# Kernel tuning notes

Measured on AMD Instinct MI355X. Metric: run time of the kernel, lower is better.

The kernel has to match this reference:

```python
import jax, jax.numpy as jnp
import numpy as np

N = 50000      # nodes
E = 640000     # edges
F_IN = 64      # node feature dim
H = 128        # hidden channels
G = 256        # graphs in batch
NEG_SLOPE = 0.2
BN_EPS = 1e-5


def setup_inputs() -> dict:
    key = jax.random.key(0)
    ks = jax.random.split(key, 32)
    rn = lambda k, shape, s=0.1: jax.random.normal(k, shape, dtype=jnp.float32) * s
    inp = {
        'x': jax.random.normal(ks[0], (N, F_IN), dtype=jnp.float32),
        'edge_index': jax.random.randint(ks[1], (2, E), 0, N, dtype=jnp.int32),
        'batch': jnp.sort(jax.random.randint(ks[2], (N,), 0, G, dtype=jnp.int32)),
        # GATConv 1
        'W1': rn(ks[3], (F_IN, H)), 'as1': rn(ks[4], (H,)), 'ad1': rn(ks[5], (H,)), 'b1': jnp.zeros((H,), jnp.float32),
        # GATConv 2
        'W2': rn(ks[6], (H, H)), 'as2': rn(ks[7], (H,)), 'ad2': rn(ks[8], (H,)), 'b2': jnp.zeros((H,), jnp.float32),
        # GATConv 3
        'W3': rn(ks[9], (H, H)), 'as3': rn(ks[10], (H,)), 'ad3': rn(ks[11], (H,)), 'b3': jnp.zeros((H,), jnp.float32),
        # BatchNorm (inference: running stats)
        'g1': jnp.ones((H,), jnp.float32), 'be1': jnp.zeros((H,), jnp.float32), 'm1': rn(ks[12], (H,), 0.01), 'v1': jnp.ones((H,), jnp.float32),
        'g2': jnp.ones((H,), jnp.float32), 'be2': jnp.zeros((H,), jnp.float32), 'm2': rn(ks[13], (H,), 0.01), 'v2': jnp.ones((H,), jnp.float32),
        'g3': jnp.ones((H,), jnp.float32), 'be3': jnp.zeros((H,), jnp.float32), 'm3': rn(ks[14], (H,), 0.01), 'v3': jnp.ones((H,), jnp.float32),
        # MLP head
        'lw1': rn(ks[15], (H, H)), 'lb1': jnp.zeros((H,), jnp.float32),
        'lw2': rn(ks[16], (H, 1)), 'lb2': jnp.zeros((1,), jnp.float32),
    }
    return inp


def gat_layer(x, src, dst, W, a_src, a_dst, b, n):
    # PyG GATConv, heads=1: linear, per-edge attention, segment softmax over dst, scatter-add.
    h = x @ W                                  # [N, H]
    s_src = h @ a_src                          # [N]
    s_dst = h @ a_dst                          # [N]
    e = jax.nn.leaky_relu(s_src[src] + s_dst[dst], NEG_SLOPE)   # [E']
    m = jax.ops.segment_max(e, dst, num_segments=n)
    ex = jnp.exp(e - m[dst])
    denom = jax.ops.segment_sum(ex, dst, num_segments=n)
    coef = ex / denom[dst]                     # softmax per destination node
    out = jax.ops.segment_sum(coef[:, None] * h[src], dst, num_segments=n)
    return out + b


def batch_norm(x, g, b, mean, var):
    return (x - mean) * jax.lax.rsqrt(var + BN_EPS) * g + b


def reference(x, edge_index, batch,
              W1, as1, ad1, b1, W2, as2, ad2, b2, W3, as3, ad3, b3,
              g1, be1, m1, v1, g2, be2, m2, v2, g3, be3, m3, v3,
              lw1, lb1, lw2, lb2):
    n = x.shape[0]
    loops = jnp.arange(n, dtype=edge_index.dtype)      # PyG adds self-loops by default
    src = jnp.concatenate([edge_index[0], loops])
    dst = jnp.concatenate([edge_index[1], loops])

    h = gat_layer(x, src, dst, W1, as1, ad1, b1, n)
    h = jax.nn.relu(batch_norm(h, g1, be1, m1, v1))
    h = gat_layer(h, src, dst, W2, as2, ad2, b2, n)
    h = jax.nn.relu(batch_norm(h, g2, be2, m2, v2))
    h = gat_layer(h, src, dst, W3, as3, ad3, b3, n)
    h = jax.nn.relu(batch_norm(h, g3, be3, m3, v3))

    # global_mean_pool
    counts = jax.ops.segment_sum(jnp.ones((n,), h.dtype), batch, num_segments=G)
    pooled = jax.ops.segment_sum(h, batch, num_segments=G) / jnp.maximum(counts, 1.0)[:, None]

    out = jax.nn.relu(pooled @ lw1 + lb1)
    out = out @ lw2 + lb2                               # [G, 1]
    return out
```

## Files before the change

kernel.cpp:

```cpp
#include <hip/hip_runtime.h>

#define HD 128
#define NEG 0.2f
#define BNEPS 1e-5f
#define BSH 11
#define NBSLOT 32

typedef unsigned int uint32;
typedef __attribute__((ext_vector_type(8))) short short8;
typedef __attribute__((ext_vector_type(4))) float floatx4;


__device__ inline float wave_sum_f(float v) {
#pragma unroll
  for (int off = 32; off; off >>= 1) v += __shfl_xor(v, off, 64);
  return v;
}
__device__ inline int wave_iscan_i(int v, int lane) {
#pragma unroll
  for (int off = 1; off < 64; off <<= 1) {
    int t = __shfl_up(v, off, 64);
    if (lane >= off) v += t;
  }
  return v;
}
__device__ inline uint32 f2bf(float f) {
  uint32 u = __float_as_uint(f);
  return (u + 0x7fffu + ((u >> 16) & 1u)) >> 16;
}
__device__ inline void kpair(int kc, int lg, int e2, bool perm, int& k_lo, int& k_hi) {
  if (!perm) {
    k_lo = kc * 32 + lg * 8 + e2 * 2;
    k_hi = k_lo + 1;
  } else {
    int w = kc * 16 + lg * 4 + e2;
    k_lo = ((w >> 4) << 5) + (w & 15);
    k_hi = k_lo + 16;
  }
}

__global__ __launch_bounds__(256)
void k_pack(const float* __restrict__ W1, const float* __restrict__ as1v,
            const float* __restrict__ ad1v, const float* __restrict__ W2,
            const float* __restrict__ as2v, const float* __restrict__ ad2v,
            const float* __restrict__ W3, const float* __restrict__ as3v,
            const float* __restrict__ ad3v,
            const float* __restrict__ b1, const float* __restrict__ g1,
            const float* __restrict__ be1, const float* __restrict__ m1,
            const float* __restrict__ v1,
            const float* __restrict__ b2, const float* __restrict__ g2,
            const float* __restrict__ be2, const float* __restrict__ m2,
            const float* __restrict__ v2,
            const float* __restrict__ b3, const float* __restrict__ g3,
            const float* __restrict__ be3, const float* __restrict__ m3,
            const float* __restrict__ v3,
            uint32* __restrict__ PW1, uint32* __restrict__ PW2,
            uint32* __restrict__ PW3, uint32* __restrict__ BFA1,
            uint32* __restrict__ BFA2, uint32* __restrict__ BFA3,
            float4* __restrict__ BNAB,
            int* __restrict__ deg32, int* __restrict__ gcnt, int n) {
  const int b = blockIdx.x, t = threadIdx.x;
  if (b >= 83) {
    const int i = (b - 83) * 256 + t;
    if (i < n * NBSLOT) deg32[i] = 0;
    if (b == 83 && t == 0) gcnt[0] = 0;
    return;
  }
  if (b < 80) {
    const float* W;
    uint32* PW;
    int KC, local;
    bool perm;
    if (b < 16) { W = W1; PW = PW1; KC = 2; perm = false; local = b; }
    else if (b < 48) { W = W2; PW = PW2; KC = 4; perm = true; local = b - 16; }
    else { W = W3; PW = PW3; KC = 4; perm = true; local = b - 48; }
    const int idx = local * 256 + t;
    const int e2 = idx & 3, l = (idx >> 2) & 63, f = idx >> 8;
    const int kc = f % KC, ct = f / KC;
    int k_lo, k_hi;
    kpair(kc, l >> 4, e2, perm, k_lo, k_hi);
    const int col = ct * 16 + (l & 15);
    PW[idx] = f2bf(W[k_lo * HD + col]) | (f2bf(W[k_hi * HD + col]) << 16);
  } else {
    const int layer = b - 80;
    const float* W = layer == 0 ? W1 : layer == 1 ? W2 : W3;
    const float* av = layer == 0 ? as1v : layer == 1 ? as2v : as3v;
    const float* dv = layer == 0 ? ad1v : layer == 1 ? ad2v : ad3v;
    const float* bb = layer == 0 ? b1 : layer == 1 ? b2 : b3;
    const float* gg = layer == 0 ? g1 : layer == 1 ? g2 : g3;
    const float* bt = layer == 0 ? be1 : layer == 1 ? be2 : be3;
    const float* mm = layer == 0 ? m1 : layer == 1 ? m2 : m3;
    const float* vv = layer == 0 ? v1 : layer == 1 ? v2 : v3;
    uint32* BFA = layer == 0 ? BFA1 : layer == 1 ? BFA2 : BFA3;
    const int K = layer == 0 ? 64 : 128, KC = K / 32;
    const bool perm = layer != 0;
    __shared__ float ws[128], wd[128];
    if (t < K) {
      float s = 0.f, d = 0.f;
      for (int j = 0; j < HD; ++j) {
        const float w = W[t * HD + j];
        s = fmaf(w, av[j], s);
        d = fmaf(w, dv[j], d);
      }
      ws[t] = s;
      wd[t] = d;
    }
    __syncthreads();
    const int total = KC * 256;
    for (int idx = t; idx < total; idx += 256) {
      const int e2 = idx & 3, l = (idx >> 2) & 63, kc = idx >> 8;
      int k_lo, k_hi;
      kpair(kc, l >> 4, e2, perm, k_lo, k_hi);
      const int li = l & 15;
      const float lo = li == 0 ? ws[k_lo] : li == 1 ? wd[k_lo] : 0.f;
      const float hi = li == 0 ? ws[k_hi] : li == 1 ? wd[k_hi] : 0.f;
      BFA[idx] = f2bf(lo) | (f2bf(hi) << 16);
    }
    if (t < 64) {
      const int c0 = (t >> 4) * 32 + (t & 15);
      const int c1 = c0 + 16;
      const float A0 = gg[c0] * rsqrtf(vv[c0] + BNEPS);
      const float A1 = gg[c1] * rsqrtf(vv[c1] + BNEPS);
      float4 r;
      r.x = A0;
      r.y = (bb[c0] - mm[c0]) * A0 + bt[c0];
      r.z = A1;
      r.w = (bb[c1] - mm[c1]) * A1 + bt[c1];
      BNAB[layer * 64 + t] = r;
    }
  }
}

__global__ __launch_bounds__(256)
void k_alloc(const int4* __restrict__ deg4, int* __restrict__ gcnt,
             int2* __restrict__ offs2, int* __restrict__ csr,
             int4* __restrict__ cursor4, int n) {
  const int t = threadIdx.x, lane = t & 63, wave = t >> 6;
  const int i = blockIdx.x * 256 + t;
  int4 q[8];
  int tot = 1;
  if (i < n) {
#pragma unroll
    for (int u = 0; u < 8; ++u) {
      q[u] = deg4[i * 8 + u];
      tot += q[u].x + q[u].y + q[u].z + q[u].w;
    }
  } else {
    tot = 0;
  }
  const int x = wave_iscan_i(tot, lane);
  __shared__ int wsum[4];
  __shared__ int bbase;
  if (lane == 63) wsum[wave] = x;
  __syncthreads();
  if (t == 0) bbase = atomicAdd(gcnt, wsum[0] + wsum[1] + wsum[2] + wsum[3]);
  __syncthreads();
  int add = bbase;
#pragma unroll
  for (int w = 0; w < 4; ++w)
    if (w < wave) add += wsum[w];
  const int start = add + x - tot;
  if (i < n) {
    csr[start] = i;
    int r = start + 1;
#pragma unroll
    for (int u = 0; u < 8; ++u) {
      int4 c;
      c.x = r; r += q[u].x;
      c.y = r; r += q[u].y;
      c.z = r; r += q[u].z;
      c.w = r; r += q[u].w;
      cursor4[i * 8 + u] = c;
    }
    offs2[i] = make_int2(start, r);
  }
}

__global__ void k_fill_edges(const int* __restrict__ src, const int* __restrict__ dst,
                             int* __restrict__ cursor, int* __restrict__ csr, int E) {
  int i = blockIdx.x * blockDim.x + threadIdx.x;
  if (i < E) {
    const int s = src[i];
    const int p = atomicAdd(&cursor[dst[i] * NBSLOT + (s >> BSH)], 1);
    csr[p] = s;
  }
}

template <int K, bool BF16IN>
__device__ inline void gemm_body(int bid, const void* __restrict__ Xv,
                                 const uint32* __restrict__ PW,
                                 const uint32* __restrict__ BFA,
                                 uint32* __restrict__ Hh, float* __restrict__ ssrc,
                                 float* __restrict__ sdst, int n) {
  constexpr int KC = K / 32;
  __shared__ uint32 Xl[64 * K / 2];
  const int t = threadIdx.x;
  const int wv = t >> 6, l = t & 63;
  const int rowbase = bid * 64;

  short8 bfr[2][KC];
#pragma unroll
  for (int c2 = 0; c2 < 2; ++c2)
#pragma unroll
    for (int kc = 0; kc < KC; ++kc)
      bfr[c2][kc] = *((const short8*)PW + ((wv * 2 + c2) * KC + kc) * 64 + l);
  short8 bfa[KC];
  if (wv == 0) {
#pragma unroll
    for (int kc = 0; kc < KC; ++kc) bfa[kc] = *((const short8*)BFA + kc * 64 + l);
  }

  if (BF16IN) {
    const uint32* Xb = (const uint32*)Xv;
#pragma unroll
    for (int B = t; B < 64 * (K / 8); B += 256) {
      const int row = B / (K / 8), cb = B % (K / 8);
      const int r = min(rowbase + row, n - 1);
      const uint4 v = *(const uint4*)&Xb[(long)r * (K / 2) + cb * 4];
      *(uint4*)&Xl[row * (K / 2) + (cb ^ (row & 7)) * 4] = v;
    }
  } else {
    const float* X = (const float*)Xv;
    for (int i = t; i < 64 * (K / 4); i += 256) {
      const int row = i / (K / 4), kq = i % (K / 4);
      const int r = min(rowbase + row, n - 1);
      const float4 v = *(const float4*)&X[(long)r * K + kq * 4];
      uint2 p;
      p.x = f2bf(v.x) | (f2bf(v.y) << 16);
      p.y = f2bf(v.z) | (f2bf(v.w) << 16);
      int byte = row * (K * 2) + kq * 8;
      byte ^= (row & 7) << 4;
      *(uint2*)((char*)Xl + byte) = p;
    }
  }
  __syncthreads();

  floatx4 acc[4][2], acc2[4];
#pragma unroll
  for (int rt = 0; rt < 4; ++rt) {
    acc[rt][0] = (floatx4){0.f, 0.f, 0.f, 0.f};
    acc[rt][1] = (floatx4){0.f, 0.f, 0.f, 0.f};
    acc2[rt] = (floatx4){0.f, 0.f, 0.f, 0.f};
  }
  const int row_l = l & 15, kgrp = l >> 4;
#pragma unroll
  for (int rt = 0; rt < 4; ++rt) {
    const int row = rt * 16 + row_l;
#pragma unroll
    for (int kc = 0; kc < KC; ++kc) {
      const int byte = (row * (K * 2) + kc * 64 + kgrp * 16) ^ ((row & 7) << 4);
      const short8 af = *(const short8*)((const char*)Xl + byte);
      acc[rt][0] = __builtin_amdgcn_mfma_f32_16x16x32_bf16(af, bfr[0][kc], acc[rt][0], 0, 0, 0);
      acc[rt][1] = __builtin_amdgcn_mfma_f32_16x16x32_bf16(af, bfr[1][kc], acc[rt][1], 0, 0, 0);
      if (wv == 0)
        acc2[rt] = __builtin_amdgcn_mfma_f32_16x16x32_bf16(af, bfa[kc], acc2[rt], 0, 0, 0);
    }
  }

#pragma unroll
  for (int rt = 0; rt < 4; ++rt) {
#pragma unroll
    for (int r = 0; r < 4; ++r) {
      const int R = rowbase + rt * 16 + kgrp * 4 + r;
      if (R < n)
        Hh[(long)R * 64 + wv * 16 + row_l] =
            f2bf(acc[rt][0][r]) | (f2bf(acc[rt][1][r]) << 16);
    }
  }
  if (wv == 0 && row_l < 2) {
    float* tgt = (row_l == 0) ? ssrc : sdst;
#pragma unroll
    for (int rt = 0; rt < 4; ++rt)
#pragma unroll
      for (int r = 0; r < 4; ++r) {
        const int R = rowbase + rt * 16 + kgrp * 4 + r;
        if (R < n) tgt[R] = acc2[rt][r];
      }
  }
}

__global__ __launch_bounds__(256)
void k_gemm1_hist(const void* __restrict__ Xv, const uint32* __restrict__ PW,
                  const uint32* __restrict__ BFA, uint32* __restrict__ Hh,
                  float* __restrict__ ssrc, float* __restrict__ sdst, int n,
                  const int* __restrict__ src, const int* __restrict__ dst,
                  int* __restrict__ deg32, int E, int GB) {
  const int b = blockIdx.x;
  if (b < GB) {
    gemm_body<64, false>(b, Xv, PW, BFA, Hh, ssrc, sdst, n);
  } else {
    const int i = (b - GB) * 256 + threadIdx.x;
    if (i < E) atomicAdd(&deg32[dst[i] * NBSLOT + (src[i] >> BSH)], 1);
  }
}

template <int K>
__global__ __launch_bounds__(256)
void k_gemm_mfma(const void* __restrict__ Xv, const uint32* __restrict__ PW,
                 const uint32* __restrict__ BFA, uint32* __restrict__ Hh,
                 float* __restrict__ ssrc, float* __restrict__ sdst, int n) {
  gemm_body<K, true>(blockIdx.x, Xv, PW, BFA, Hh, ssrc, sdst, n);
}

__global__ __launch_bounds__(256)
void k_agg(const uint32* __restrict__ Hh, const float* __restrict__ ssrc,
           const float* __restrict__ sdst, const int2* __restrict__ offs2,
           const int* __restrict__ csr, const float4* __restrict__ BNAB,
           uint32* __restrict__ Ybf, int n) {
  const int wid = (blockIdx.x * blockDim.x + threadIdx.x) >> 6;
  const int lane = threadIdx.x & 63;
  if (wid >= n) return;
  const int2 se = offs2[wid];
  const float sdv = sdst[wid];
  float acc0 = 0.f, acc1 = 0.f, denom = 0.f;
  for (int base = se.x; base < se.y; base += 64) {
    const int m = min(64, se.y - base);
    int sidx = 0;
    float p = 0.f;
    if (lane < m) {
      sidx = csr[base + lane];
      const float tt = ssrc[sidx] + sdv;
      const float e = (tt > 0.f) ? tt : NEG * tt;
      p = __expf(e);
    }
    denom += wave_sum_f(p);
    const uint32 pu = __float_as_uint(p);
    for (int jj = 0; jj < m; jj += 16) {
      uint32 g[16];
#pragma unroll
      for (int u = 0; u < 16; ++u) {
        if (jj + u < m) {
          const int s = __builtin_amdgcn_readlane(sidx, jj + u);
          g[u] = Hh[(long)s * 64 + lane];
        }
      }
#pragma unroll
      for (int u = 0; u < 16; ++u) {
        if (jj + u < m) {
          const float w = __uint_as_float(__builtin_amdgcn_readlane(pu, jj + u));
          acc0 = fmaf(w, __uint_as_float(g[u] << 16), acc0);
          acc1 = fmaf(w, __uint_as_float(g[u] & 0xffff0000u), acc1);
        }
      }
    }
  }
  const float inv = 1.f / denom;
  const float4 ab = BNAB[lane];
  const float v0 = fmaxf(fmaf(acc0 * inv, ab.x, ab.y), 0.f);
  const float v1 = fmaxf(fmaf(acc1 * inv, ab.z, ab.w), 0.f);
  Ybf[(long)wid * 64 + lane] = f2bf(v0) | (f2bf(v1) << 16);
}

__global__ __launch_bounds__(256)
void k_pool_head(const uint32* __restrict__ Ybf, const int* __restrict__ batch, int n,
                 const float* __restrict__ lw1, const float* __restrict__ lb1,
                 const float* __restrict__ lw2, const float* __restrict__ lb2,
                 float* __restrict__ out) {
  const int g = blockIdx.x;
  const int wave = threadIdx.x >> 6, lane = threadIdx.x & 63;
  int lo = 0, hi = n;
  while (lo < hi) { int mid = (lo + hi) >> 1; if (batch[mid] < g) lo = mid + 1; else hi = mid; }
  const int start = lo;
  hi = n;
  while (lo < hi) { int mid = (lo + hi) >> 1; if (batch[mid] < g + 1) lo = mid + 1; else hi = mid; }
  const int end = lo;
  const int c0 = (lane >> 4) * 32 + (lane & 15);
  const int c1 = c0 + 16;
  float m0 = 0.f, m1 = 0.f;
  for (int i = start + wave; i < end; i += 4) {
    const uint32 gv = Ybf[(long)i * 64 + lane];
    m0 += __uint_as_float(gv << 16);
    m1 += __uint_as_float(gv & 0xffff0000u);
  }
  __shared__ float red[4][HD];
  red[wave][c0] = m0;
  red[wave][c1] = m1;
  __syncthreads();
  if (wave == 0) {
    m0 = red[0][c0] + red[1][c0] + red[2][c0] + red[3][c0];
    m1 = red[0][c1] + red[1][c1] + red[2][c1] + red[3][c1];
    const float cnt = (float)(end - start);
    const float invc = (cnt > 0.f) ? 1.f / cnt : 0.f;
    m0 *= invc;
    m1 *= invc;
    float t0 = lb1[c0], t1 = lb1[c1];
    for (int k = 0; k < HD; ++k) {
      const int srcl = ((k >> 5) << 4) + (k & 15);
      const float pv = __shfl(((k >> 4) & 1) ? m1 : m0, srcl, 64);
      t0 = fmaf(pv, lw1[k * HD + c0], t0);
      t1 = fmaf(pv, lw1[k * HD + c1], t1);
    }
    t0 = fmaxf(t0, 0.f);
    t1 = fmaxf(t1, 0.f);
    float p = t0 * lw2[c0] + t1 * lw2[c1];
#pragma unroll
    for (int off = 32; off; off >>= 1) p += __shfl_xor(p, off, 64);
    if (lane == 0) out[g] = p + lb2[0];
  }
}


extern "C" void kernel_launch(void* const* d_in, const int* in_sizes, int n_in,
                              void* d_out, int out_size, void* d_ws, size_t ws_size,
                              hipStream_t stream) {
  const float* x = (const float*)d_in[0];
  const int* ei = (const int*)d_in[1];
  const int* batch = (const int*)d_in[2];
  const float* W1 = (const float*)d_in[3];
  const float* as1 = (const float*)d_in[4];
  const float* ad1 = (const float*)d_in[5];
  const float* b1 = (const float*)d_in[6];
  const float* W2 = (const float*)d_in[7];
  const float* as2 = (const float*)d_in[8];
  const float* ad2 = (const float*)d_in[9];
  const float* b2 = (const float*)d_in[10];
  const float* W3 = (const float*)d_in[11];
  const float* as3 = (const float*)d_in[12];
  const float* ad3 = (const float*)d_in[13];
  const float* b3 = (const float*)d_in[14];
  const float* g1 = (const float*)d_in[15];
  const float* be1 = (const float*)d_in[16];
  const float* m1 = (const float*)d_in[17];
  const float* v1 = (const float*)d_in[18];
  const float* g2 = (const float*)d_in[19];
  const float* be2 = (const float*)d_in[20];
  const float* m2 = (const float*)d_in[21];
  const float* v2 = (const float*)d_in[22];
  const float* g3 = (const float*)d_in[23];
  const float* be3 = (const float*)d_in[24];
  const float* m3 = (const float*)d_in[25];
  const float* v3 = (const float*)d_in[26];
  const float* lw1 = (const float*)d_in[27];
  const float* lb1 = (const float*)d_in[28];
  const float* lw2 = (const float*)d_in[29];
  const float* lb2 = (const float*)d_in[30];

  const int n = in_sizes[0] / 64;
  const int E = in_sizes[1] / 2;
  const int* src = ei;
  const int* dst = ei + E;

  uint32* hbuf = (uint32*)d_ws;
  uint32* ybuf = hbuf + (long)n * 64;
  float* ssrc = (float*)(ybuf + (long)n * 64);
  float* sdstv = ssrc + n;
  int* deg32 = (int*)(sdstv + n);
  int2* offs2 = (int2*)(deg32 + (long)n * NBSLOT);
  int* cursor = (int*)(offs2 + n);
  int* csr = cursor + (long)n * NBSLOT;
  int* gcnt = csr + (E + n);
  uint32* PW1 = (uint32*)(gcnt + 4);
  uint32* PW2 = PW1 + 4096;
  uint32* PW3 = PW2 + 8192;
  uint32* BFA1 = PW3 + 8192;
  uint32* BFA2 = BFA1 + 512;
  uint32* BFA3 = BFA2 + 1024;
  float4* BNAB = (float4*)(BFA3 + 1024);

  const int B = 256;
  dim3 blk(B);
  const int nb = (n + B - 1) / B;
  const int eb = (E + B - 1) / B;
  const int zb = ((n * NBSLOT) + B - 1) / B;
  const int GB = (n + 63) / 64;

  k_pack<<<dim3(83 + zb), blk, 0, stream>>>(
      W1, as1, ad1, W2, as2, ad2, W3, as3, ad3,
      b1, g1, be1, m1, v1, b2, g2, be2, m2, v2, b3, g3, be3, m3, v3,
      PW1, PW2, PW3, BFA1, BFA2, BFA3, BNAB, deg32, gcnt, n);
  k_gemm1_hist<<<dim3(GB + eb), blk, 0, stream>>>(x, PW1, BFA1, hbuf, ssrc, sdstv, n,
                                                  src, dst, deg32, E, GB);
  k_alloc<<<dim3(nb), blk, 0, stream>>>((const int4*)deg32, gcnt, offs2, csr,
                                        (int4*)cursor, n);
  k_fill_edges<<<dim3(eb), blk, 0, stream>>>(src, dst, cursor, csr, E);

  const dim3 agrid((n + 3) / 4);
  k_agg<<<agrid, blk, 0, stream>>>(hbuf, ssrc, sdstv, offs2, csr, BNAB + 0, ybuf, n);
  k_gemm_mfma<128><<<dim3(GB), blk, 0, stream>>>(ybuf, PW2, BFA2, hbuf, ssrc, sdstv, n);
  k_agg<<<agrid, blk, 0, stream>>>(hbuf, ssrc, sdstv, offs2, csr, BNAB + 64, ybuf, n);
  k_gemm_mfma<128><<<dim3(GB), blk, 0, stream>>>(ybuf, PW3, BFA3, hbuf, ssrc, sdstv, n);
  k_agg<<<agrid, blk, 0, stream>>>(hbuf, ssrc, sdstv, offs2, csr, BNAB + 128, ybuf, n);
  k_pool_head<<<dim3(256), blk, 0, stream>>>(ybuf, batch, n, lw1, lb1, lw2, lb2,
                                             (float*)d_out);
}
```

Before: 229.3 us.

## Gather two edges per wave with 8-byte loads; split pooling into atomic partials plus head

The aggregation kernel now has each half-wave gather a different neighbor row with 8-byte loads, so one load instruction covers two edges. The two halves' partial sums are combined with a cross-half shuffle before BN/ReLU and the bf16 store. Mean pooling is split into 4 blocks per graph that atomically add into a zeroed pooled buffer, followed by a separate small head kernel. This aims to raise memory-level parallelism in the gather and to use more blocks in pooling, at the cost of an extra launch and float atomics.

```diff
diff --git a/kernel.cpp b/kernel.cpp
--- a/kernel.cpp
+++ b/kernel.cpp
@@ -57,12 +57,14 @@
             uint32* __restrict__ PW1, uint32* __restrict__ PW2,
             uint32* __restrict__ PW3, uint32* __restrict__ BFA1,
             uint32* __restrict__ BFA2, uint32* __restrict__ BFA3,
-            float4* __restrict__ BNAB,
-            int* __restrict__ deg32, int* __restrict__ gcnt, int n) {
+            float4* __restrict__ BNAB, int* __restrict__ deg32,
+            int* __restrict__ gcnt, float* __restrict__ pooled, int G, int n) {
   const int b = blockIdx.x, t = threadIdx.x;
   if (b >= 83) {
     const int i = (b - 83) * 256 + t;
-    if (i < n * NBSLOT) deg32[i] = 0;
+    const int ZD = n * NBSLOT;
+    if (i < ZD) deg32[i] = 0;
+    else if (i < ZD + G * HD) pooled[i - ZD] = 0.f;
     if (b == 83 && t == 0) gcnt[0] = 0;
     return;
   }
@@ -312,7 +314,9 @@
   if (wid >= n) return;
   const int2 se = offs2[wid];
   const float sdv = sdst[wid];
-  float acc0 = 0.f, acc1 = 0.f, denom = 0.f;
+  const bool lohalf = lane < 32;
+  const int lw = (lane & 31) * 2;
+  float a0 = 0.f, a1 = 0.f, a2 = 0.f, a3 = 0.f, denom = 0.f;
   for (int base = se.x; base < se.y; base += 64) {
     const int m = min(64, se.y - base);
     int sidx = 0;
@@ -325,49 +329,65 @@
     }
     denom += wave_sum_f(p);
     const uint32 pu = __float_as_uint(p);
-    for (int jj = 0; jj < m; jj += 16) {
-      uint32 g[16];
-#pragma unroll
-      for (int u = 0; u < 16; ++u) {
-        if (jj + u < m) {
-          const int s = __builtin_amdgcn_readlane(sidx, jj + u);
-          g[u] = Hh[(long)s * 64 + lane];
-        }
+    const int npairs = (m + 1) >> 1;
+    for (int j0 = 0; j0 < npairs; j0 += 8) {
+      uint2 g[8];
+#pragma unroll
+      for (int u = 0; u < 8; ++u) {
+        const int k2 = (j0 + u) * 2;
+        const int sa = __builtin_amdgcn_readlane(sidx, k2);
+        const int sb = __builtin_amdgcn_readlane(sidx, k2 + 1);
+        const int sm = lohalf ? sa : sb;
+        g[u] = *(const uint2*)&Hh[(long)sm * 64 + lw];
       }
 #pragma unroll
-      for (int u = 0; u < 16; ++u) {
-        if (jj + u < m) {
-          const float w = __uint_as_float(__builtin_amdgcn_readlane(pu, jj + u));
-          acc0 = fmaf(w, __uint_as_float(g[u] << 16), acc0);
-          acc1 = fmaf(w, __uint_as_float(g[u] & 0xffff0000u), acc1);
-        }
+      for (int u = 0; u < 8; ++u) {
+        const int k2 = (j0 + u) * 2;
+        const float wa = __uint_as_float(__builtin_amdgcn_readlane(pu, k2));
+        const float wb = __uint_as_float(__builtin_amdgcn_readlane(pu, k2 + 1));
+        const float wm = lohalf ? wa : wb;
+        a0 = fmaf(wm, __uint_as_float(g[u].x << 16), a0);
+        a1 = fmaf(wm, __uint_as_float(g[u].x & 0xffff0000u), a1);
+        a2 = fmaf(wm, __uint_as_float(g[u].y << 16), a2);
+        a3 = fmaf(wm, __uint_as_float(g[u].y & 0xffff0000u), a3);
       }
     }
   }
-  const float inv = 1.f / denom;
-  const float4 ab = BNAB[lane];
-  const float v0 = fmaxf(fmaf(acc0 * inv, ab.x, ab.y), 0.f);
-  const float v1 = fmaxf(fmaf(acc1 * inv, ab.z, ab.w), 0.f);
-  Ybf[(long)wid * 64 + lane] = f2bf(v0) | (f2bf(v1) << 16);
-}
-
-__global__ __launch_bounds__(256)
-void k_pool_head(const uint32* __restrict__ Ybf, const int* __restrict__ batch, int n,
-                 const float* __restrict__ lw1, const float* __restrict__ lb1,
-                 const float* __restrict__ lw2, const float* __restrict__ lb2,
-                 float* __restrict__ out) {
-  const int g = blockIdx.x;
+  a0 += __shfl_xor(a0, 32, 64);
+  a1 += __shfl_xor(a1, 32, 64);
+  a2 += __shfl_xor(a2, 32, 64);
+  a3 += __shfl_xor(a3, 32, 64);
+  if (lane < 32) {
+    const float inv = 1.f / denom;
+    const float4 ab0 = BNAB[lw];
+    const float4 ab1 = BNAB[lw + 1];
+    const float v0 = fmaxf(fmaf(a0 * inv, ab0.x, ab0.y), 0.f);
+    const float v1 = fmaxf(fmaf(a1 * inv, ab0.z, ab0.w), 0.f);
+    const float v2 = fmaxf(fmaf(a2 * inv, ab1.x, ab1.y), 0.f);
+    const float v3 = fmaxf(fmaf(a3 * inv, ab1.z, ab1.w), 0.f);
+    uint2 o;
+    o.x = f2bf(v0) | (f2bf(v1) << 16);
+    o.y = f2bf(v2) | (f2bf(v3) << 16);
+    *(uint2*)&Ybf[(long)wid * 64 + lw] = o;
+  }
+}
+
+__global__ __launch_bounds__(256)
+void k_pool_part(const uint32* __restrict__ Ybf, const int* __restrict__ batch,
+                 int n, float* __restrict__ pooled) {
+  const int g = blockIdx.x >> 2, q = blockIdx.x & 3;
   const int wave = threadIdx.x >> 6, lane = threadIdx.x & 63;
   int lo = 0, hi = n;
   while (lo < hi) { int mid = (lo + hi) >> 1; if (batch[mid] < g) lo = mid + 1; else hi = mid; }
   const int start = lo;
   hi = n;
   while (lo < hi) { int mid = (lo + hi) >> 1; if (batch[mid] < g + 1) lo = mid + 1; else hi = mid; }
-  const int end = lo;
-  const int c0 = (lane >> 4) * 32 + (lane & 15);
-  const int c1 = c0 + 16;
+  const int len = lo - start;
+  const int qs = start + (len * q) / 4;
+  const int qe = start + (len * (q + 1)) / 4;
+  const int c0 = (lane >> 4) * 32 + (lane & 15), c1 = c0 + 16;
   float m0 = 0.f, m1 = 0.f;
-  for (int i = start + wave; i < end; i += 4) {
+  for (int i = qs + wave; i < qe; i += 4) {
     const uint32 gv = Ybf[(long)i * 64 + lane];
     m0 += __uint_as_float(gv << 16);
     m1 += __uint_as_float(gv & 0xffff0000u);
@@ -379,24 +399,42 @@
   if (wave == 0) {
     m0 = red[0][c0] + red[1][c0] + red[2][c0] + red[3][c0];
     m1 = red[0][c1] + red[1][c1] + red[2][c1] + red[3][c1];
-    const float cnt = (float)(end - start);
-    const float invc = (cnt > 0.f) ? 1.f / cnt : 0.f;
-    m0 *= invc;
-    m1 *= invc;
-    float t0 = lb1[c0], t1 = lb1[c1];
-    for (int k = 0; k < HD; ++k) {
-      const int srcl = ((k >> 5) << 4) + (k & 15);
-      const float pv = __shfl(((k >> 4) & 1) ? m1 : m0, srcl, 64);
-      t0 = fmaf(pv, lw1[k * HD + c0], t0);
-      t1 = fmaf(pv, lw1[k * HD + c1], t1);
-    }
-    t0 = fmaxf(t0, 0.f);
-    t1 = fmaxf(t1, 0.f);
-    float p = t0 * lw2[c0] + t1 * lw2[c1];
-#pragma unroll
-    for (int off = 32; off; off >>= 1) p += __shfl_xor(p, off, 64);
-    if (lane == 0) out[g] = p + lb2[0];
-  }
+    atomicAdd(&pooled[g * HD + c0], m0);
+    atomicAdd(&pooled[g * HD + c1], m1);
+  }
+}
+
+__global__ __launch_bounds__(256)
+void k_head(const float* __restrict__ pooled, const int* __restrict__ batch, int n,
+            int G, const float* __restrict__ lw1, const float* __restrict__ lb1,
+            const float* __restrict__ lw2, const float* __restrict__ lb2,
+            float* __restrict__ out) {
+  const int g = blockIdx.x * 4 + (threadIdx.x >> 6);
+  const int lane = threadIdx.x & 63;
+  if (g >= G) return;
+  int lo = 0, hi = n;
+  while (lo < hi) { int mid = (lo + hi) >> 1; if (batch[mid] < g) lo = mid + 1; else hi = mid; }
+  const int start = lo;
+  hi = n;
+  while (lo < hi) { int mid = (lo + hi) >> 1; if (batch[mid] < g + 1) lo = mid + 1; else hi = mid; }
+  const int cnt = lo - start;
+  const float invc = (cnt > 0) ? 1.f / (float)cnt : 0.f;
+  const int c0 = (lane >> 4) * 32 + (lane & 15), c1 = c0 + 16;
+  const float m0 = pooled[g * HD + c0] * invc;
+  const float m1 = pooled[g * HD + c1] * invc;
+  float t0 = lb1[c0], t1 = lb1[c1];
+  for (int k = 0; k < HD; ++k) {
+    const int srcl = ((k >> 5) << 4) + (k & 15);
+    const float pv = __shfl(((k >> 4) & 1) ? m1 : m0, srcl, 64);
+    t0 = fmaf(pv, lw1[k * HD + c0], t0);
+    t1 = fmaf(pv, lw1[k * HD + c1], t1);
+  }
+  t0 = fmaxf(t0, 0.f);
+  t1 = fmaxf(t1, 0.f);
+  float p = t0 * lw2[c0] + t1 * lw2[c1];
+#pragma unroll
+  for (int off = 32; off; off >>= 1) p += __shfl_xor(p, off, 64);
+  if (lane == 0) out[g] = p + lb2[0];
 }
 
 
@@ -437,6 +475,7 @@
 
   const int n = in_sizes[0] / 64;
   const int E = in_sizes[1] / 2;
+  const int G = out_size;
   const int* src = ei;
   const int* dst = ei + E;
 
@@ -456,18 +495,19 @@
   uint32* BFA2 = BFA1 + 512;
   uint32* BFA3 = BFA2 + 1024;
   float4* BNAB = (float4*)(BFA3 + 1024);
+  float* pooled = (float*)(BNAB + 3 * 64);
 
   const int B = 256;
   dim3 blk(B);
   const int nb = (n + B - 1) / B;
   const int eb = (E + B - 1) / B;
-  const int zb = ((n * NBSLOT) + B - 1) / B;
+  const int zb = (n * NBSLOT + G * HD + B - 1) / B;
   const int GB = (n + 63) / 64;
 
   k_pack<<<dim3(83 + zb), blk, 0, stream>>>(
       W1, as1, ad1, W2, as2, ad2, W3, as3, ad3,
       b1, g1, be1, m1, v1, b2, g2, be2, m2, v2, b3, g3, be3, m3, v3,
-      PW1, PW2, PW3, BFA1, BFA2, BFA3, BNAB, deg32, gcnt, n);
+      PW1, PW2, PW3, BFA1, BFA2, BFA3, BNAB, deg32, gcnt, pooled, G, n);
   k_gemm1_hist<<<dim3(GB + eb), blk, 0, stream>>>(x, PW1, BFA1, hbuf, ssrc, sdstv, n,
                                                   src, dst, deg32, E, GB);
   k_alloc<<<dim3(nb), blk, 0, stream>>>((const int4*)deg32, gcnt, offs2, csr,
@@ -480,6 +520,7 @@
   k_agg<<<agrid, blk, 0, stream>>>(hbuf, ssrc, sdstv, offs2, csr, BNAB + 64, ybuf, n);
   k_gemm_mfma<128><<<dim3(GB), blk, 0, stream>>>(ybuf, PW3, BFA3, hbuf, ssrc, sdstv, n);
   k_agg<<<agrid, blk, 0, stream>>>(hbuf, ssrc, sdstv, offs2, csr, BNAB + 128, ybuf, n);
-  k_pool_head<<<dim3(256), blk, 0, stream>>>(ybuf, batch, n, lw1, lb1, lw2, lb2,
-                                             (float*)d_out);
-}
+  k_pool_part<<<dim3(4 * G), blk, 0, stream>>>(ybuf, batch, n, pooled);
+  k_head<<<dim3((G + 3) / 4), blk, 0, stream>>>(pooled, batch, n, G, lw1, lb1, lw2,
+                                                lb2, (float*)d_out);
+}
```

After: 245.2 us. 6.9% more time.

## Drop source-bucketed CSR slots and split pooling into parallel partial sums

Applied to the files above, without the earlier changes.

Replaces the 32-slot per-destination degree/cursor arrays, which grouped sources by high bits, with a single degree and cursor per node. This removes zeroing and scanning of n*32 ints and the int4 cursor writes. The price is that CSR neighbour order within a destination is no longer grouped by source range, which may hurt gather locality in aggregation. Pooling is also split across 4 blocks per graph that atomically accumulate into a zeroed buffer, with the MLP head moved to a separate small kernel.

```diff
diff --git a/kernel.cpp b/kernel.cpp
--- a/kernel.cpp
+++ b/kernel.cpp
@@ -3,8 +3,6 @@
 #define HD 128
 #define NEG 0.2f
 #define BNEPS 1e-5f
-#define BSH 11
-#define NBSLOT 32
 
 typedef unsigned int uint32;
 typedef __attribute__((ext_vector_type(8))) short short8;
@@ -57,12 +55,13 @@
             uint32* __restrict__ PW1, uint32* __restrict__ PW2,
             uint32* __restrict__ PW3, uint32* __restrict__ BFA1,
             uint32* __restrict__ BFA2, uint32* __restrict__ BFA3,
-            float4* __restrict__ BNAB,
-            int* __restrict__ deg32, int* __restrict__ gcnt, int n) {
+            float4* __restrict__ BNAB, int* __restrict__ deg,
+            int* __restrict__ gcnt, float* __restrict__ pooled, int G, int n) {
   const int b = blockIdx.x, t = threadIdx.x;
   if (b >= 83) {
     const int i = (b - 83) * 256 + t;
-    if (i < n * NBSLOT) deg32[i] = 0;
+    if (i < n) deg[i] = 0;
+    else if (i < n + G * HD) pooled[i - n] = 0.f;
     if (b == 83 && t == 0) gcnt[0] = 0;
     return;
   }
@@ -132,23 +131,13 @@
 }
 
 __global__ __launch_bounds__(256)
-void k_alloc(const int4* __restrict__ deg4, int* __restrict__ gcnt,
+void k_alloc(const int* __restrict__ deg, int* __restrict__ gcnt,
              int2* __restrict__ offs2, int* __restrict__ csr,
-             int4* __restrict__ cursor4, int n) {
+             int* __restrict__ cursor, int n) {
   const int t = threadIdx.x, lane = t & 63, wave = t >> 6;
   const int i = blockIdx.x * 256 + t;
-  int4 q[8];
-  int tot = 1;
-  if (i < n) {
-#pragma unroll
-    for (int u = 0; u < 8; ++u) {
-      q[u] = deg4[i * 8 + u];
-      tot += q[u].x + q[u].y + q[u].z + q[u].w;
-    }
-  } else {
-    tot = 0;
-  }
-  const int x = wave_iscan_i(tot, lane);
+  const int v = (i < n) ? deg[i] + 1 : 0;
+  const int x = wave_iscan_i(v, lane);
   __shared__ int wsum[4];
   __shared__ int bbase;
   if (lane == 63) wsum[wave] = x;
@@ -159,31 +148,18 @@
 #pragma unroll
   for (int w = 0; w < 4; ++w)
     if (w < wave) add += wsum[w];
-  const int start = add + x - tot;
+  const int start = add + x - v;
   if (i < n) {
     csr[start] = i;
-    int r = start + 1;
-#pragma unroll
-    for (int u = 0; u < 8; ++u) {
-      int4 c;
-      c.x = r; r += q[u].x;
-      c.y = r; r += q[u].y;
-      c.z = r; r += q[u].z;
-      c.w = r; r += q[u].w;
-      cursor4[i * 8 + u] = c;
-    }
-    offs2[i] = make_int2(start, r);
+    cursor[i] = start + 1;
+    offs2[i] = make_int2(start, start + v);
   }
 }
 
 __global__ void k_fill_edges(const int* __restrict__ src, const int* __restrict__ dst,
                              int* __restrict__ cursor, int* __restrict__ csr, int E) {
   int i = blockIdx.x * blockDim.x + threadIdx.x;
-  if (i < E) {
-    const int s = src[i];
-    const int p = atomicAdd(&cursor[dst[i] * NBSLOT + (s >> BSH)], 1);
-    csr[p] = s;
-  }
+  if (i < E) { int p = atomicAdd(&cursor[dst[i]], 1); csr[p] = src[i]; }
 }
 
 template <int K, bool BF16IN>
@@ -283,14 +259,13 @@
 void k_gemm1_hist(const void* __restrict__ Xv, const uint32* __restrict__ PW,
                   const uint32* __restrict__ BFA, uint32* __restrict__ Hh,
                   float* __restrict__ ssrc, float* __restrict__ sdst, int n,
-                  const int* __restrict__ src, const int* __restrict__ dst,
-                  int* __restrict__ deg32, int E, int GB) {
+                  const int* __restrict__ dst, int* __restrict__ deg, int E, int GB) {
   const int b = blockIdx.x;
   if (b < GB) {
     gemm_body<64, false>(b, Xv, PW, BFA, Hh, ssrc, sdst, n);
   } else {
     const int i = (b - GB) * 256 + threadIdx.x;
-    if (i < E) atomicAdd(&deg32[dst[i] * NBSLOT + (src[i] >> BSH)], 1);
+    if (i < E) atomicAdd(&deg[dst[i]], 1);
   }
 }
 
@@ -352,22 +327,21 @@
 }
 
 __global__ __launch_bounds__(256)
-void k_pool_head(const uint32* __restrict__ Ybf, const int* __restrict__ batch, int n,
-                 const float* __restrict__ lw1, const float* __restrict__ lb1,
-                 const float* __restrict__ lw2, const float* __restrict__ lb2,
-                 float* __restrict__ out) {
-  const int g = blockIdx.x;
+void k_pool_part(const uint32* __restrict__ Ybf, const int* __restrict__ batch,
+                 int n, float* __restrict__ pooled) {
+  const int g = blockIdx.x >> 2, q = blockIdx.x & 3;
   const int wave = threadIdx.x >> 6, lane = threadIdx.x & 63;
   int lo = 0, hi = n;
   while (lo < hi) { int mid = (lo + hi) >> 1; if (batch[mid] < g) lo = mid + 1; else hi = mid; }
   const int start = lo;
   hi = n;
   while (lo < hi) { int mid = (lo + hi) >> 1; if (batch[mid] < g + 1) lo = mid + 1; else hi = mid; }
-  const int end = lo;
-  const int c0 = (lane >> 4) * 32 + (lane & 15);
-  const int c1 = c0 + 16;
+  const int len = lo - start;
+  const int qs = start + (len * q) / 4;
+  const int qe = start + (len * (q + 1)) / 4;
+  const int c0 = (lane >> 4) * 32 + (lane & 15), c1 = c0 + 16;
   float m0 = 0.f, m1 = 0.f;
-  for (int i = start + wave; i < end; i += 4) {
+  for (int i = qs + wave; i < qe; i += 4) {
     const uint32 gv = Ybf[(long)i * 64 + lane];
     m0 += __uint_as_float(gv << 16);
     m1 += __uint_as_float(gv & 0xffff0000u);
@@ -379,24 +353,42 @@
   if (wave == 0) {
     m0 = red[0][c0] + red[1][c0] + red[2][c0] + red[3][c0];
     m1 = red[0][c1] + red[1][c1] + red[2][c1] + red[3][c1];
-    const float cnt = (float)(end - start);
-    const float invc = (cnt > 0.f) ? 1.f / cnt : 0.f;
-    m0 *= invc;
-    m1 *= invc;
-    float t0 = lb1[c0], t1 = lb1[c1];
-    for (int k = 0; k < HD; ++k) {
-      const int srcl = ((k >> 5) << 4) + (k & 15);
-      const float pv = __shfl(((k >> 4) & 1) ? m1 : m0, srcl, 64);
-      t0 = fmaf(pv, lw1[k * HD + c0], t0);
-      t1 = fmaf(pv, lw1[k * HD + c1], t1);
-    }
-    t0 = fmaxf(t0, 0.f);
-    t1 = fmaxf(t1, 0.f);
-    float p = t0 * lw2[c0] + t1 * lw2[c1];
-#pragma unroll
-    for (int off = 32; off; off >>= 1) p += __shfl_xor(p, off, 64);
-    if (lane == 0) out[g] = p + lb2[0];
-  }
+    atomicAdd(&pooled[g * HD + c0], m0);
+    atomicAdd(&pooled[g * HD + c1], m1);
+  }
+}
+
+__global__ __launch_bounds__(256)
+void k_head(const float* __restrict__ pooled, const int* __restrict__ batch, int n,
+            int G, const float* __restrict__ lw1, const float* __restrict__ lb1,
+            const float* __restrict__ lw2, const float* __restrict__ lb2,
+            float* __restrict__ out) {
+  const int g = blockIdx.x * 4 + (threadIdx.x >> 6);
+  const int lane = threadIdx.x & 63;
+  if (g >= G) return;
+  int lo = 0, hi = n;
+  while (lo < hi) { int mid = (lo + hi) >> 1; if (batch[mid] < g) lo = mid + 1; else hi = mid; }
+  const int start = lo;
+  hi = n;
+  while (lo < hi) { int mid = (lo + hi) >> 1; if (batch[mid] < g + 1) lo = mid + 1; else hi = mid; }
+  const int cnt = lo - start;
+  const float invc = (cnt > 0) ? 1.f / (float)cnt : 0.f;
+  const int c0 = (lane >> 4) * 32 + (lane & 15), c1 = c0 + 16;
+  const float m0 = pooled[g * HD + c0] * invc;
+  const float m1 = pooled[g * HD + c1] * invc;
+  float t0 = lb1[c0], t1 = lb1[c1];
+  for (int k = 0; k < HD; ++k) {
+    const int srcl = ((k >> 5) << 4) + (k & 15);
+    const float pv = __shfl(((k >> 4) & 1) ? m1 : m0, srcl, 64);
+    t0 = fmaf(pv, lw1[k * HD + c0], t0);
+    t1 = fmaf(pv, lw1[k * HD + c1], t1);
+  }
+  t0 = fmaxf(t0, 0.f);
+  t1 = fmaxf(t1, 0.f);
+  float p = t0 * lw2[c0] + t1 * lw2[c1];
+#pragma unroll
+  for (int off = 32; off; off >>= 1) p += __shfl_xor(p, off, 64);
+  if (lane == 0) out[g] = p + lb2[0];
 }
 
 
@@ -437,6 +429,7 @@
 
   const int n = in_sizes[0] / 64;
   const int E = in_sizes[1] / 2;
+  const int G = out_size;
   const int* src = ei;
   const int* dst = ei + E;
 
@@ -444,10 +437,10 @@
   uint32* ybuf = hbuf + (long)n * 64;
   float* ssrc = (float*)(ybuf + (long)n * 64);
   float* sdstv = ssrc + n;
-  int* deg32 = (int*)(sdstv + n);
-  int2* offs2 = (int2*)(deg32 + (long)n * NBSLOT);
+  int* deg = (int*)(sdstv + n);
+  int2* offs2 = (int2*)(deg + n);
   int* cursor = (int*)(offs2 + n);
-  int* csr = cursor + (long)n * NBSLOT;
+  int* csr = cursor + n;
   int* gcnt = csr + (E + n);
   uint32* PW1 = (uint32*)(gcnt + 4);
   uint32* PW2 = PW1 + 4096;
@@ -456,22 +449,22 @@
   uint32* BFA2 = BFA1 + 512;
   uint32* BFA3 = BFA2 + 1024;
   float4* BNAB = (float4*)(BFA3 + 1024);
+  float* pooled = (float*)(BNAB + 3 * 64);
 
   const int B = 256;
   dim3 blk(B);
   const int nb = (n + B - 1) / B;
   const int eb = (E + B - 1) / B;
-  const int zb = ((n * NBSLOT) + B - 1) / B;
+  const int zb = (n + G * HD + B - 1) / B;
   const int GB = (n + 63) / 64;
 
   k_pack<<<dim3(83 + zb), blk, 0, stream>>>(
       W1, as1, ad1, W2, as2, ad2, W3, as3, ad3,
       b1, g1, be1, m1, v1, b2, g2, be2, m2, v2, b3, g3, be3, m3, v3,
-      PW1, PW2, PW3, BFA1, BFA2, BFA3, BNAB, deg32, gcnt, n);
+      PW1, PW2, PW3, BFA1, BFA2, BFA3, BNAB, deg, gcnt, pooled, G, n);
   k_gemm1_hist<<<dim3(GB + eb), blk, 0, stream>>>(x, PW1, BFA1, hbuf, ssrc, sdstv, n,
-                                                  src, dst, deg32, E, GB);
-  k_alloc<<<dim3(nb), blk, 0, stream>>>((const int4*)deg32, gcnt, offs2, csr,
-                                        (int4*)cursor, n);
+                                                  dst, deg, E, GB);
+  k_alloc<<<dim3(nb), blk, 0, stream>>>(deg, gcnt, offs2, csr, cursor, n);
   k_fill_edges<<<dim3(eb), blk, 0, stream>>>(src, dst, cursor, csr, E);
 
   const dim3 agrid((n + 3) / 4);
@@ -480,6 +473,7 @@
   k_agg<<<agrid, blk, 0, stream>>>(hbuf, ssrc, sdstv, offs2, csr, BNAB + 64, ybuf, n);
   k_gemm_mfma<128><<<dim3(GB), blk, 0, stream>>>(ybuf, PW3, BFA3, hbuf, ssrc, sdstv, n);
   k_agg<<<agrid, blk, 0, stream>>>(hbuf, ssrc, sdstv, offs2, csr, BNAB + 128, ybuf, n);
-  k_pool_head<<<dim3(256), blk, 0, stream>>>(ybuf, batch, n, lw1, lb1, lw2, lb2,
-                                             (float*)d_out);
-}
+  k_pool_part<<<dim3(4 * G), blk, 0, stream>>>(ybuf, batch, n, pooled);
+  k_head<<<dim3((G + 3) / 4), blk, 0, stream>>>(pooled, batch, n, G, lw1, lb1, lw2,
+                                                lb2, (float*)d_out);
+}
```

Result: no change. 225.9 us (median of 2 runs) (-1.5%).
